# Optimization experiments

Measured on AMD Instinct MI355X. Metric: run time of the kernel, lower is better.

Reference implementation:

```python
import jax, jax.numpy as jnp
import numpy as np

DEG = [1, 72, 201, 816, 1790, 3756, 6923, 12768, 20286, 31710, 51623, 82296, 124280, 177576, 251115, 326064, 395760, 456840, 506179, 516200, 507003, 493746, 489256, 453936, 420025, 411320, 427761, 420700, 420500, 426780, 414284, 407008, 394053, 360910, 322245, 313704, 282902, 270940, 237783, 209000, 193766, 177870, 162110, 144848, 121230, 112700, 93483, 88512, 72275, 80700, 68799, 56784, 42665, 30996, 25630, 12936, 9804, 8584, 5251, 3480, 3111, 2728, 1890, 1472, 1235, 330, 201, 68, 69, 0, 71]
_d = np.array(DEG, dtype=np.float64)
AVG_LOG = float((np.log(np.arange(len(_d)) + 1.0) * _d).sum() / _d.sum())  # avg_deg['log']

N_NODES, N_EDGES, N_GRAPHS = 10000, 100000, 64
TOWERS, F, F_OUT, N_LAYERS = 5, 75, 15, 4


def setup_inputs() -> dict:
    key = jax.random.key(0)
    ks = jax.random.split(key, 32)
    r = lambda i, shape: jax.random.normal(ks[i], shape, jnp.float32) * 0.1
    return {
        "x": jax.random.normal(ks[0], (N_NODES, 14), jnp.float32),
        "edge_index": jax.random.randint(ks[1], (2, N_EDGES), 0, N_NODES, dtype=jnp.int32),
        "edge_attr": jax.random.normal(ks[2], (N_EDGES, 4), jnp.float32),
        "batch": jnp.sort(jax.random.randint(ks[3], (N_NODES,), 0, N_GRAPHS, dtype=jnp.int32)),
        "node_emb_w": r(4, (14, F)), "node_emb_b": r(5, (F,)),
        "edge_emb_w": r(6, (4, 50)), "edge_emb_b": r(7, (50,)),
        "ee_w": r(8, (N_LAYERS, 50, F)), "ee_b": r(9, (N_LAYERS, F)),
        "pre_w": r(10, (N_LAYERS, TOWERS, 3 * F, F)), "pre_b": r(11, (N_LAYERS, TOWERS, F)),
        "post_w": r(12, (N_LAYERS, TOWERS, 13 * F, F_OUT)), "post_b": r(13, (N_LAYERS, TOWERS, F_OUT)),
        "lin_w": r(14, (N_LAYERS, F, F)), "lin_b": r(15, (N_LAYERS, F)),
        "bn_g": jnp.ones((N_LAYERS, F), jnp.float32), "bn_b": jnp.zeros((N_LAYERS, F), jnp.float32),
        "mlp_w1": r(16, (F, 50)), "mlp_b1": r(17, (50,)),
        "mlp_w2": r(18, (50, 25)), "mlp_b2": r(19, (25,)),
        "mlp_w3": r(20, (25, 1)), "mlp_b3": r(21, (1,)),
    }


def _pna_conv(x, src, dst, ea, ee_w, ee_b, pre_w, pre_b, post_w, post_b, lin_w, lin_b):
    # x: [N, F]; ea: [E, edge_dim]; divide_input=False so every tower sees full F.
    N = x.shape[0]
    e = ea @ ee_w + ee_b                                   # edge_encoder  [E, F]
    h = jnp.concatenate([x[dst], x[src], e], axis=-1)       # [x_i, x_j, e] [E, 3F]
    m = jnp.einsum('ef,tfg->etg', h, pre_w) + pre_b         # per-tower pre nn [E, T, F]
    cnt = jax.ops.segment_sum(jnp.ones((m.shape[0],), x.dtype), dst, N)  # in-degree [N]
    cnt1 = jnp.maximum(cnt, 1.0)[:, None, None]
    mean = jax.ops.segment_sum(m, dst, N) / cnt1
    mean_sq = jax.ops.segment_sum(m * m, dst, N) / cnt1
    std = jnp.sqrt(jax.nn.relu(mean_sq - mean * mean) + 1e-5)
    has = (cnt > 0)[:, None, None]
    mn = jnp.where(has, jax.ops.segment_min(m, dst, N), 0.0)
    mx = jnp.where(has, jax.ops.segment_max(m, dst, N), 0.0)
    agg = jnp.concatenate([mean, mn, mx, std], axis=-1)     # [N, T, 4F]
    scl = jnp.log(cnt1 + 1.0) / AVG_LOG                     # amplification scaler
    out = jnp.concatenate([agg, agg * scl, agg / scl], -1)  # identity/amp/atten [N, T, 12F]
    x_rep = jnp.broadcast_to(x[:, None, :], (N, TOWERS, x.shape[1]))
    out = jnp.concatenate([x_rep, out], axis=-1)            # [N, T, 13F]
    out = jnp.einsum('ntf,tfg->ntg', out, post_w) + post_b  # per-tower post nn [N, T, F_out]
    return out.reshape(N, -1) @ lin_w + lin_b               # [N, F]


def _bn(x, g, b):
    mu = x.mean(0)
    var = x.var(0)  # biased, as torch BatchNorm1d uses for normalization
    return (x - mu) * jax.lax.rsqrt(var + 1e-5) * g + b


def reference(x, edge_index, edge_attr, batch, node_emb_w, node_emb_b, edge_emb_w, edge_emb_b,
              ee_w, ee_b, pre_w, pre_b, post_w, post_b, lin_w, lin_b, bn_g, bn_b,
              mlp_w1, mlp_b1, mlp_w2, mlp_b2, mlp_w3, mlp_b3):
    src, dst = edge_index[0], edge_index[1]
    h = x @ node_emb_w + node_emb_b
    ea = edge_attr @ edge_emb_w + edge_emb_b
    for i in range(N_LAYERS):
        h = jax.nn.relu(_bn(_pna_conv(h, src, dst, ea, ee_w[i], ee_b[i], pre_w[i], pre_b[i],
                                      post_w[i], post_b[i], lin_w[i], lin_b[i]), bn_g[i], bn_b[i]))
    per_atom = h
    g = jax.ops.segment_sum(h, batch, N_GRAPHS)             # global_add_pool [G, F]
    g = jax.nn.relu(g @ mlp_w1 + mlp_b1)
    g = jax.nn.relu(g @ mlp_w2 + mlp_b2)
    g = (g @ mlp_w3 + mlp_b3).reshape(-1)                   # num_out==1 -> view(-1)
    return (g, per_atom)
```

## Files before the change

### kernel.cpp

```cpp
#include <hip/hip_runtime.h>
#include <math.h>

#define NN 10000
#define NE 100000
#define NGR 64
#define NT 5
#define FD 75
#define FOUT 15
#define NLAY 4
#define MAXB 1792

typedef __bf16 bf16;
typedef __bf16 bf16x8 __attribute__((ext_vector_type(8)));
typedef float f32x4 __attribute__((ext_vector_type(4)));

__device__ inline unsigned pk2(float a, float b) {
  bf16 x = (bf16)a, y = (bf16)b;
  unsigned short ux, uy;
  __builtin_memcpy(&ux, &x, 2); __builtin_memcpy(&uy, &y, 2);
  return (unsigned)ux | ((unsigned)uy << 16);
}


__global__ __launch_bounds__(256) void k_node_emb(const float* __restrict__ x,
    const float* __restrict__ w, const float* __restrict__ b, bf16* __restrict__ hbf) {
  int idx = blockIdx.x * 256 + threadIdx.x;
  if (idx >= NN * FD) return;
  int n = idx / FD, f = idx - n * FD;
  float acc = b[f];
#pragma unroll
  for (int k = 0; k < 14; ++k) acc += x[n * 14 + k] * w[k * FD + f];
  hbf[n * 80 + f] = (bf16)acc;
}

__global__ __launch_bounds__(256) void k_edge_emb(const float* __restrict__ eattr,
    const float* __restrict__ w, const float* __restrict__ b, bf16* __restrict__ eabf) {
  int idx = blockIdx.x * 256 + threadIdx.x;
  if (idx >= NE * 50) return;
  int e = idx / 50, c = idx - e * 50;
  float acc = b[c];
#pragma unroll
  for (int k = 0; k < 4; ++k) acc += eattr[e * 4 + k] * w[k * 50 + c];
  eabf[e * 56 + c] = (bf16)acc;
}

__global__ __launch_bounds__(256) void k_count(const int* __restrict__ dst, int* __restrict__ deg) {
  int e = blockIdx.x * 256 + threadIdx.x;
  if (e < NE) atomicAdd(&deg[dst[e]], 1);
}

__global__ __launch_bounds__(1024) void k_scan(const int* __restrict__ deg, int* __restrict__ rowptr) {
  __shared__ int buf[1024];
  __shared__ int carry;
  int tid = threadIdx.x;
  if (tid == 0) carry = 0;
  __syncthreads();
  for (int base = 0; base < NN; base += 1024) {
    int i = base + tid;
    int v = (i < NN) ? deg[i] : 0;
    buf[tid] = v;
    __syncthreads();
    for (int off = 1; off < 1024; off <<= 1) {
      int t = (tid >= off) ? buf[tid - off] : 0;
      __syncthreads();
      buf[tid] += t;
      __syncthreads();
    }
    int inc = buf[tid];
    int tot = buf[1023];
    if (i < NN) rowptr[i + 1] = carry + inc;
    __syncthreads();
    if (tid == 0) carry += tot;
    __syncthreads();
  }
  if (tid == 0) rowptr[0] = 0;
}

__global__ __launch_bounds__(256) void k_scl(const int* __restrict__ deg, float* __restrict__ scl,
                                             float* __restrict__ iscl, float inv_avg_log) {
  int n = blockIdx.x * 256 + threadIdx.x;
  if (n >= NN) return;
  float c1 = fmaxf((float)deg[n], 1.f);
  float s = logf(c1 + 1.f) * inv_avg_log;
  scl[n] = s;
  iscl[n] = 1.f / s;
}

__global__ __launch_bounds__(256) void k_scatter(const int* __restrict__ dst, const int* __restrict__ rowptr,
    int* __restrict__ cursor, int* __restrict__ eids) {
  int e = blockIdx.x * 256 + threadIdx.x;
  if (e >= NE) return;
  int d = dst[e];
  int pos = rowptr[d] + atomicAdd(&cursor[d], 1);
  eids[pos] = e;
}

__global__ __launch_bounds__(256) void k_next(const int* __restrict__ rowptr, int* __restrict__ nxt) {
  int n = blockIdx.x * 256 + threadIdx.x;
  if (n >= NN) return;
  int base = rowptr[n];
  int lo = n + 1, hi = min(n + 128, NN);
  while (lo < hi) {
    int mid = (lo + hi + 1) >> 1;
    if (rowptr[mid] - base <= 128) lo = mid; else hi = mid - 1;
  }
  nxt[n] = lo;
}

__global__ __launch_bounds__(1024) void k_walk(const int* __restrict__ nxt,
    int* __restrict__ bstart, int* __restrict__ nblk) {
  __shared__ int lnx[NN];
  int tid = threadIdx.x;
  for (int i = tid; i < NN; i += 1024) lnx[i] = nxt[i];
  __syncthreads();
  if (tid == 0) {
    int b = 0, n = 0;
    while (n < NN && b < MAXB) { bstart[b++] = n; n = lnx[n]; }
    bstart[b] = NN;
    nblk[0] = b;
  }
}


__global__ __launch_bounds__(256) void k_combine(const float* __restrict__ pre_w,
    const float* __restrict__ pre_b, const float* __restrict__ ee_w, const float* __restrict__ ee_b,
    bf16* __restrict__ Wct, float* __restrict__ bc) {
  int idx = blockIdx.x * 256 + threadIdx.x;
  if (idx >= 384 * 256) return;
  int c = idx >> 8, s = idx & 255;
  int t = c / 75, g = c - t * 75;
  int chunk = s >> 6, within = s & 63, sblk = within >> 3, elem = within & 7;
  int lb = sblk ^ (c & 7);
  int k = chunk * 64 + lb * 8 + elem;
  float v = 0.f;
  if (c < 375) {
    if (k < 75)                    v = pre_w[(t * 225 + k) * 75 + g];
    else if (k >= 80 && k < 155)   v = pre_w[(t * 225 + 75 + (k - 80)) * 75 + g];
    else if (k >= 160 && k < 210) {
      int kk = k - 160;
      float a = 0.f;
      for (int f2 = 0; f2 < 75; ++f2) a += ee_w[kk * 75 + f2] * pre_w[(t * 225 + 150 + f2) * 75 + g];
      v = a;
    }
  }
  Wct[c * 256 + s] = (bf16)v;
  if (s == 0) {
    float a = 0.f;
    if (c < 375) {
      a = pre_b[t * 75 + g];
      for (int f2 = 0; f2 < 75; ++f2) a += ee_b[f2] * pre_w[(t * 225 + 150 + f2) * 75 + g];
    }
    bc[c] = a;
  }
}

__global__ __launch_bounds__(256) void k_PL(const float* __restrict__ pw,
    const float* __restrict__ lw, float* __restrict__ PL) {
  int idx = blockIdx.x * 256 + threadIdx.x;
  if (idx >= 5 * 975 * 80) return;
  int t = idx / (975 * 80), rem = idx - t * 975 * 80;
  int row = rem / 80, o = rem - row * 80;
  float v = 0.f;
  if (o < 75) {
#pragma unroll
    for (int j = 0; j < 15; ++j)
      v += pw[((size_t)t * 975 + row) * 15 + j] * lw[(t * 15 + j) * 75 + o];
  }
  PL[idx] = v;
}

__global__ __launch_bounds__(256) void k_combine2b(const float* __restrict__ PL,
    bf16* __restrict__ Wct2) {
  int idx = blockIdx.x * 256 + threadIdx.x;
  if (idx >= 256 * 1664) return;
  int c = idx / 1664, s = idx - c * 1664;
  int chunk = s >> 6, within = s & 63, sblk = within >> 3, elem = within & 7;
  int lb = sblk ^ (c & 7);
  int k = chunk * 64 + lb * 8 + elem;
  int g2 = c / 80, o = c - g2 * 80;
  float val = 0.f;
  if (c < 240 && o < 75) {
    if (k < 75) {
      if (g2 == 0) {
#pragma unroll
        for (int t = 0; t < 5; ++t) val += PL[(t * 975 + k) * 80 + o];
      }
    } else if (k >= 80 && k < 1616) {
      int q = k - 80;
      int si = q / 384, cc = q - si * 384;
      if (cc < 375) {
        int t = cc / 75, g = cc - t * 75;
        int row = 75 + g2 * 300 + si * 75 + g;
        val = PL[((size_t)t * 975 + row) * 80 + o];
      }
    }
  }
  Wct2[(size_t)c * 1664 + s] = (bf16)val;
}

__global__ __launch_bounds__(128) void k_zbias(const float* __restrict__ pb,
    const float* __restrict__ lw, const float* __restrict__ lb, float* __restrict__ zb) {
  int o = blockIdx.x * 128 + threadIdx.x;
  if (o >= 80) return;
  float val = 0.f;
  if (o < 75) {
    val = lb[o];
    for (int t = 0; t < 5; ++t)
      for (int j = 0; j < 15; ++j)
        val += pb[t * 15 + j] * lw[(t * 15 + j) * 75 + o];
  }
  zb[o] = val;
}


#define APTR_(g_, pd_, ps_, pe_) \
  ((g_) < 10 ? (pd_) + (g_) * 8 : (g_) < 20 ? (ps_) + ((g_) - 10) * 8 : \
   (g_) < 27 ? (pe_) + ((g_) - 20) * 8 : zerobuf)

#define LOADA(c_) do { int g_ = (c_) * 8 + slb;                \
    pa0 = *(const uint4*)APTR_(g_, pd0, ps0, pe0);             \
    pa1 = *(const uint4*)APTR_(g_, pd1, ps1, pe1);             \
    pa2 = *(const uint4*)APTR_(g_, pd2, ps2, pe2);             \
    pa3 = *(const uint4*)APTR_(g_, pd3, ps3, pe3); } while (0)

#define LOADB(ntb_, c_) do {                                                      \
    const bf16* wp_ = Wct + (size_t)((ntb_) + sr) * 256 + (c_) * 64 + slb * 8;    \
    pq0 = *(const uint4*)(wp_ + 0 * 8192);                                        \
    pq1 = *(const uint4*)(wp_ + 1 * 8192);                                        \
    pq2 = *(const uint4*)(wp_ + 2 * 8192);                                        \
    pq3 = *(const uint4*)(wp_ + 3 * 8192); } while (0)

#define STORE_AB() do { int swz_ = (slb ^ (sr & 7)) << 4;       \
    *(uint4*)(As + (0 * 32 + sr) * 128 + swz_) = pa0;           \
    *(uint4*)(As + (1 * 32 + sr) * 128 + swz_) = pa1;           \
    *(uint4*)(As + (2 * 32 + sr) * 128 + swz_) = pa2;           \
    *(uint4*)(As + (3 * 32 + sr) * 128 + swz_) = pa3;           \
    *(uint4*)(Bs + (0 * 32 + sr) * 128 + (slb << 4)) = pq0;     \
    *(uint4*)(Bs + (1 * 32 + sr) * 128 + (slb << 4)) = pq1;     \
    *(uint4*)(Bs + (2 * 32 + sr) * 128 + (slb << 4)) = pq2;     \
    *(uint4*)(Bs + (3 * 32 + sr) * 128 + (slb << 4)) = pq3; } while (0)

__global__ __launch_bounds__(256) void k_pre_fused(
    const bf16* __restrict__ hbf, const bf16* __restrict__ eabf,
    const int* __restrict__ eids, const int* __restrict__ srcA, const int* __restrict__ dstA,
    const int* __restrict__ rowptr, const int* __restrict__ bstart, const int* __restrict__ nblk,
    const bf16* __restrict__ Wct, const float* __restrict__ bc,
    const bf16* __restrict__ zerobuf, bf16* __restrict__ aggbf2) {
  __shared__ __align__(16) unsigned char smem[33792];
  unsigned char* As = smem;
  unsigned char* Bs = smem + 16384;
  bf16* m_lds = (bf16*)smem;
  __shared__ const bf16* pDl[128];
  __shared__ const bf16* pSl[128];
  __shared__ const bf16* pEl[128];
  __shared__ int nodeRows[129];
  __shared__ int nq[5];

  const int b = blockIdx.x;
  if (b >= nblk[0]) return;
  const int ntb = blockIdx.y * 128;
  const int tid = threadIdx.x;
  const int n0b = bstart[b], n1b = bstart[b + 1];
  const int rbase = rowptr[n0b];
  const int nrows = rowptr[n1b] - rbase;
  const int nnod = n1b - n0b;

  if (tid == 0) { nq[0] = 0; nq[1] = 0; nq[2] = 0; nq[3] = 0; nq[4] = nnod; }
  if (tid < 128) {
    if (tid < nrows) {
      int e = eids[rbase + tid];
      pDl[tid] = hbf + dstA[e] * 80;
      pSl[tid] = hbf + srcA[e] * 80;
      pEl[tid] = eabf + e * 56;
    } else { pDl[tid] = zerobuf; pSl[tid] = zerobuf; pEl[tid] = zerobuf; }
  }
  if (tid <= nnod) nodeRows[tid] = rowptr[n0b + tid] - rbase;
  __syncthreads();
  if (tid < nnod) {
#pragma unroll
    for (int q = 1; q <= 3; ++q) {
      int target = (nrows * q) >> 2;
      if (nodeRows[tid] < target && nodeRows[tid + 1] >= target) nq[q] = tid + 1;
    }
  }

  const int lane = tid & 63;
  const int wave = tid >> 6;
  const int wr = wave >> 1, wc = wave & 1;
  const int l15 = lane & 15, l4 = lane >> 4;
  const int sr = tid >> 3, slb = tid & 7;

  const bf16 *pd0 = pDl[sr],      *ps0 = pSl[sr],      *pe0 = pEl[sr];
  const bf16 *pd1 = pDl[32 + sr], *ps1 = pSl[32 + sr], *pe1 = pEl[32 + sr];
  const bf16 *pd2 = pDl[64 + sr], *ps2 = pSl[64 + sr], *pe2 = pEl[64 + sr];
  const bf16 *pd3 = pDl[96 + sr], *ps3 = pSl[96 + sr], *pe3 = pEl[96 + sr];

  f32x4 acc[4][4];
  f32x4 zv = {0.f, 0.f, 0.f, 0.f};
#pragma unroll
  for (int i = 0; i < 4; ++i)
#pragma unroll
    for (int j = 0; j < 4; ++j) acc[i][j] = zv;

  uint4 pa0, pa1, pa2, pa3, pq0, pq1, pq2, pq3;
  LOADA(0); LOADB(ntb, 0);

#pragma unroll
  for (int c = 0; c < 4; ++c) {
    STORE_AB();
    __syncthreads();
    if (c < 3) { LOADA(c + 1); LOADB(ntb, c + 1); }
#pragma unroll
    for (int kk = 0; kk < 2; ++kk) {
      int kb = kk * 4 + l4;
      bf16x8 af[4], bfv[4];
#pragma unroll
      for (int i = 0; i < 4; ++i) {
        int row = wr * 64 + i * 16 + l15;
        af[i] = *(const bf16x8*)(As + row * 128 + ((kb ^ (row & 7)) << 4));
      }
#pragma unroll
      for (int j = 0; j < 4; ++j) {
        int col = wc * 64 + j * 16 + l15;
        bfv[j] = *(const bf16x8*)(Bs + col * 128 + ((kb ^ (col & 7)) << 4));
      }
#pragma unroll
      for (int i = 0; i < 4; ++i)
#pragma unroll
        for (int j = 0; j < 4; ++j)
          acc[i][j] = __builtin_amdgcn_mfma_f32_16x16x32_bf16(af[i], bfv[j], acc[i][j], 0, 0, 0);
    }
    __syncthreads();
  }

  float bcv[4];
#pragma unroll
  for (int j = 0; j < 4; ++j) bcv[j] = bc[ntb + wc * 64 + j * 16 + l15];
#pragma unroll
  for (int i = 0; i < 4; ++i) {
    int R = wr * 64 + i * 16 + l4 * 4;
#pragma unroll
    for (int j = 0; j < 4; ++j) {
      int col = wc * 64 + j * 16 + l15;
#pragma unroll
      for (int q = 0; q < 4; ++q)
        m_lds[(R + q) * 132 + col] = (bf16)(acc[i][j][q] + bcv[j]);
    }
  }
  __syncthreads();

  {
    const int cp = tid & 63;
    const int qq = tid >> 6;
    const unsigned char* mb = (const unsigned char*)m_lds;
    for (int i = nq[qq]; i < nq[qq + 1]; ++i) {
      int ra = nodeRows[i], rb2 = nodeRows[i + 1];
      float s0 = 0.f, q0 = 0.f, a0 = INFINITY, b0 = -INFINITY;
      float s1 = 0.f, q1 = 0.f, a1 = INFINITY, b1 = -INFINITY;
      for (int r = ra; r < rb2; ++r) {
        unsigned u = *(const unsigned*)(mb + r * 264 + cp * 4);
        float v0 = __uint_as_float(u << 16);
        float v1 = __uint_as_float(u & 0xffff0000u);
        s0 += v0; q0 += v0 * v0; a0 = fminf(a0, v0); b0 = fmaxf(b0, v0);
        s1 += v1; q1 += v1 * v1; a1 = fminf(a1, v1); b1 = fmaxf(b1, v1);
      }
      int d = rb2 - ra;
      float inv = 1.f / ((d > 0) ? (float)d : 1.f);
      float m0 = s0 * inv, m1 = s1 * inv;
      float sd0 = sqrtf(fmaxf(q0 * inv - m0 * m0, 0.f) + 1e-5f);
      float sd1 = sqrtf(fmaxf(q1 * inv - m1 * m1, 0.f) + 1e-5f);
      if (d == 0) { a0 = 0.f; b0 = 0.f; a1 = 0.f; b1 = 0.f; }
      bf16* ag = aggbf2 + (size_t)(n0b + i) * 1536 + ntb + cp * 2;
      *(unsigned*)(ag)        = pk2(m0, m1);
      *(unsigned*)(ag + 384)  = pk2(a0, a1);
      *(unsigned*)(ag + 768)  = pk2(b0, b1);
      *(unsigned*)(ag + 1152) = pk2(sd0, sd1);
    }
  }
}


#define APG_(g_) ((nA >= NN || (g_) >= 202) ? zerobuf : \
    ((g_) < 10 ? hbf + nA * 80 + (g_) * 8 : aggbf2 + (size_t)nA * 1536 + ((g_) - 10) * 8))

#define LOADP4(c_) do {                                                 \
    int gA_ = (c_) * 16 + slb;                                          \
    pa0 = *(const uint4*)APG_(gA_);                                     \
    pa1 = *(const uint4*)APG_(gA_ + 8);                                 \
    int ko_ = (c_) * 128 + slb * 8;                                     \
    pb0 = *(const uint4*)(pc0 + ko_);                                   \
    pb1 = *(const uint4*)(pc0 + ko_ + 64);                              \
    pb2 = *(const uint4*)(pc1 + ko_);                                   \
    pb3 = *(const uint4*)(pc1 + ko_ + 64);                              \
    pb4 = *(const uint4*)(pc2 + ko_);                                   \
    pb5 = *(const uint4*)(pc2 + ko_ + 64);                              \
    pb6 = *(const uint4*)(pc3 + ko_);                                   \
    pb7 = *(const uint4*)(pc3 + ko_ + 64);                              \
  } while (0)

__global__ __launch_bounds__(256) void k_post4(const bf16* __restrict__ hbf,
    const bf16* __restrict__ aggbf2, const bf16* __restrict__ Wct2,
    const float* __restrict__ zb, const float* __restrict__ scl, const float* __restrict__ iscl,
    const bf16* __restrict__ zerobuf, float* __restrict__ z, float* __restrict__ stat_raw_l) {
  __shared__ __align__(16) unsigned char smem[40960];
  unsigned char* As = smem;
  unsigned char* Bs = smem + 8192;
  float* Ps = (float*)smem;
  __shared__ float sclS[32], isclS[32];
  const int n0 = blockIdx.x * 32;
  const int y  = blockIdx.y;
  const int tid = threadIdx.x;
  const int lane = tid & 63, wave = tid >> 6;
  const int l15 = lane & 15, l4 = lane >> 4;
  const int sr = tid >> 3, slb = tid & 7;
  const int nA = n0 + sr;

  const bf16 *pc0, *pc1, *pc2, *pc3;
  {
    int c0 = sr, c1 = sr + 32, c2 = sr + 64, c3 = sr + 96;
    int l0 = (c0 / 40) * 80 + y * 40 + (c0 % 40);
    int l1 = (c1 / 40) * 80 + y * 40 + (c1 % 40);
    int l2 = (c2 / 40) * 80 + y * 40 + (c2 % 40);
    int l3 = (c3 < 120) ? ((c3 / 40) * 80 + y * 40 + (c3 % 40)) : 0;
    pc0 = Wct2 + (size_t)l0 * 1664;
    pc1 = Wct2 + (size_t)l1 * 1664;
    pc2 = Wct2 + (size_t)l2 * 1664;
    pc3 = Wct2 + (size_t)l3 * 1664;
  }
  if (tid < 32) {
    int n = n0 + tid;
    sclS[tid] = (n < NN) ? scl[n] : 0.f;
    isclS[tid] = (n < NN) ? iscl[n] : 0.f;
  }

  f32x4 acc[2][2];
  f32x4 zvv = {0.f, 0.f, 0.f, 0.f};
#pragma unroll
  for (int i = 0; i < 2; ++i)
#pragma unroll
    for (int j = 0; j < 2; ++j) acc[i][j] = zvv;

  uint4 pa0, pa1, pb0, pb1, pb2, pb3, pb4, pb5, pb6, pb7;
  LOADP4(0);
  for (int c = 0; c < 13; ++c) {
    {
      int s1_ = (slb ^ (sr & 7)) << 4;
      *(uint4*)(As + sr * 256 + s1_) = pa0;
      *(uint4*)(As + sr * 256 + s1_ + 128) = pa1;
      *(uint4*)(Bs + (sr)      * 256 + (slb << 4)) = pb0;
      *(uint4*)(Bs + (sr)      * 256 + (slb << 4) + 128) = pb1;
      *(uint4*)(Bs + (sr + 32) * 256 + (slb << 4)) = pb2;
      *(uint4*)(Bs + (sr + 32) * 256 + (slb << 4) + 128) = pb3;
      *(uint4*)(Bs + (sr + 64) * 256 + (slb << 4)) = pb4;
      *(uint4*)(Bs + (sr + 64) * 256 + (slb << 4) + 128) = pb5;
      *(uint4*)(Bs + (sr + 96) * 256 + (slb << 4)) = pb6;
      *(uint4*)(Bs + (sr + 96) * 256 + (slb << 4) + 128) = pb7;
    }
    __syncthreads();
    if (c < 12) LOADP4(c + 1);
#pragma unroll
    for (int kk = 0; kk < 4; ++kk) {
      int kb = kk * 4 + l4;
      bf16x8 af[2], bv[2];
#pragma unroll
      for (int i = 0; i < 2; ++i) {
        int row = i * 16 + l15;
        af[i] = *(const bf16x8*)(As + row * 256 + (((kb & 8) | ((kb & 7) ^ (row & 7))) << 4));
      }
#pragma unroll
      for (int j = 0; j < 2; ++j) {
        int cidx = wave * 32 + j * 16 + l15;
        bv[j] = *(const bf16x8*)(Bs + cidx * 256 + (((kb & 8) | ((kb & 7) ^ (cidx & 7))) << 4));
      }
#pragma unroll
      for (int i = 0; i < 2; ++i)
#pragma unroll
        for (int j = 0; j < 2; ++j)
          acc[i][j] = __builtin_amdgcn_mfma_f32_16x16x32_bf16(af[i], bv[j], acc[i][j], 0, 0, 0);
    }
    __syncthreads();
  }

#pragma unroll
  for (int i = 0; i < 2; ++i) {
#pragma unroll
    for (int j = 0; j < 2; ++j) {
      int cidx = wave * 32 + j * 16 + l15;
#pragma unroll
      for (int q = 0; q < 4; ++q)
        Ps[(i * 16 + l4 * 4 + q) * 132 + cidx] = acc[i][j][q];
    }
  }
  __syncthreads();

  float v0_, v1_, v2_, v3_, v4_;
  int r0_, r1_, r2_, r3_, r4_, f0_, f1_, f2_, f3_, f4_;
#define EPI(t_, vv_, rr_, ff_) do {                                           \
    int idx_ = tid + (t_) * 256;                                              \
    rr_ = idx_ / 40; ff_ = idx_ - rr_ * 40;                                   \
    int n_ = n0 + rr_, zc_ = y * 40 + ff_;                                    \
    float v_ = 0.f;                                                           \
    if (n_ < NN && zc_ < 75) {                                                \
      v_ = Ps[rr_ * 132 + ff_] + sclS[rr_] * Ps[rr_ * 132 + 40 + ff_]         \
         + isclS[rr_] * Ps[rr_ * 132 + 80 + ff_] + zb[zc_];                   \
      z[n_ * 75 + zc_] = v_;                                                  \
    }                                                                         \
    vv_ = v_;                                                                 \
  } while (0)
  EPI(0, v0_, r0_, f0_); EPI(1, v1_, r1_, f1_); EPI(2, v2_, r2_, f2_);
  EPI(3, v3_, r3_, f3_); EPI(4, v4_, r4_, f4_);
#undef EPI
  __syncthreads();
  Ps[r0_ * 132 + f0_] = v0_;
  Ps[r1_ * 132 + f1_] = v1_;
  Ps[r2_ * 132 + f2_] = v2_;
  Ps[r3_ * 132 + f3_] = v3_;
  Ps[r4_ * 132 + f4_] = v4_;
  __syncthreads();
  if (tid < 40) {
    int zc = y * 40 + tid;
    if (zc < 75) {
      float s = 0.f, s2 = 0.f;
#pragma unroll
      for (int r = 0; r < 32; ++r) {
        float v = Ps[r * 132 + tid];
        s += v; s2 += v * v;
      }
      atomicAdd(&stat_raw_l[zc], s);
      atomicAdd(&stat_raw_l[75 + zc], s2);
    }
  }
}

__global__ __launch_bounds__(256) void k_bnapply(const float* __restrict__ z,
    const float* __restrict__ stat_raw, const float* __restrict__ g, const float* __restrict__ b,
    float* __restrict__ outF, bf16* __restrict__ hbf) {
  int idx = blockIdx.x * 256 + threadIdx.x;
  if (idx >= NN * FD) return;
  int n = idx / FD, f = idx - n * FD;
  float mu = stat_raw[f] * (1.f / NN);
  float var = stat_raw[75 + f] * (1.f / NN) - mu * mu;
  var = fmaxf(var, 0.f);
  float rs = 1.f / sqrtf(var + 1e-5f);
  float v = (z[idx] - mu) * rs * g[f] + b[f];
  v = fmaxf(v, 0.f);
  if (outF) outF[idx] = v;
  hbf[n * 80 + f] = (bf16)v;
}

__global__ __launch_bounds__(256) void k_pool(const float* __restrict__ h, const int* __restrict__ batch,
                                              float* __restrict__ gpool) {
  int idx = blockIdx.x * 256 + threadIdx.x;
  if (idx >= NN * FD) return;
  int n = idx / FD, f = idx - n * FD;
  atomicAdd(&gpool[batch[n] * FD + f], h[idx]);
}

__global__ __launch_bounds__(256) void k_mlp(const float* __restrict__ gpool,
    const float* __restrict__ w1, const float* __restrict__ b1,
    const float* __restrict__ w2, const float* __restrict__ b2,
    const float* __restrict__ w3, const float* __restrict__ b3,
    float* __restrict__ out) {
  __shared__ float G[NGR * FD];
  __shared__ float G1[NGR * 50];
  __shared__ float G2[NGR * 25];
  int tid = threadIdx.x;
  for (int i = tid; i < NGR * FD; i += 256) G[i] = gpool[i];
  __syncthreads();
  for (int i = tid; i < NGR * 50; i += 256) {
    int r = i / 50, c = i - r * 50;
    float a = b1[c];
    for (int k = 0; k < FD; ++k) a += G[r * FD + k] * w1[k * 50 + c];
    G1[i] = fmaxf(a, 0.f);
  }
  __syncthreads();
  for (int i = tid; i < NGR * 25; i += 256) {
    int r = i / 25, c = i - r * 25;
    float a = b2[c];
    for (int k = 0; k < 50; ++k) a += G1[r * 50 + k] * w2[k * 25 + c];
    G2[i] = fmaxf(a, 0.f);
  }
  __syncthreads();
  if (tid < NGR) {
    float a = b3[0];
    for (int k = 0; k < 25; ++k) a += G2[tid * 25 + k] * w3[k];
    out[tid] = a;
  }
}


extern "C" void kernel_launch(void* const* d_in, const int* in_sizes, int n_in,
                              void* d_out, int out_size, void* d_ws, size_t ws_size,
                              hipStream_t stream) {
  (void)in_sizes; (void)n_in; (void)out_size; (void)ws_size;
  const float* x      = (const float*)d_in[0];
  const int*   eidx   = (const int*)  d_in[1];
  const float* eattr  = (const float*)d_in[2];
  const int*   batch  = (const int*)  d_in[3];
  const float* nw     = (const float*)d_in[4];
  const float* nb     = (const float*)d_in[5];
  const float* ew     = (const float*)d_in[6];
  const float* ebias  = (const float*)d_in[7];
  const float* ee_w   = (const float*)d_in[8];
  const float* ee_b   = (const float*)d_in[9];
  const float* pre_w  = (const float*)d_in[10];
  const float* pre_b  = (const float*)d_in[11];
  const float* post_w = (const float*)d_in[12];
  const float* post_b = (const float*)d_in[13];
  const float* lin_w  = (const float*)d_in[14];
  const float* lin_b  = (const float*)d_in[15];
  const float* bn_g   = (const float*)d_in[16];
  const float* bn_b   = (const float*)d_in[17];
  const float* w1 = (const float*)d_in[18];
  const float* b1 = (const float*)d_in[19];
  const float* w2 = (const float*)d_in[20];
  const float* b2 = (const float*)d_in[21];
  const float* w3 = (const float*)d_in[22];
  const float* b3 = (const float*)d_in[23];

  const int* srcA = eidx;
  const int* dstA = eidx + NE;

  char* base = (char*)d_ws;
  size_t off = 0;
  auto alloc = [&](size_t bytes) -> char* {
    char* p = base + off;
    off = (off + bytes + 255) & ~(size_t)255;
    return p;
  };
  bf16*  hbf    = (bf16*) alloc((size_t)NN * 80 * 2);
  bf16*  eabf   = (bf16*) alloc((size_t)NE * 56 * 2);
  bf16*  aggbf2 = (bf16*) alloc((size_t)NN * 1536 * 2);
  float* z      = (float*)alloc((size_t)NN * FD * 4);
  bf16*  WctA   = (bf16*) alloc((size_t)NLAY * 384 * 256 * 2);
  float* bcA    = (float*)alloc((size_t)NLAY * 384 * 4);
  bf16*  Wct2A  = (bf16*) alloc((size_t)NLAY * 256 * 1664 * 2);
  float* zbA    = (float*)alloc((size_t)NLAY * 80 * 4);
  float* PL     = (float*)alloc((size_t)5 * 975 * 80 * 4);
  float* scl    = (float*)alloc(NN * 4);
  float* iscl   = (float*)alloc(NN * 4);
  int*   deg    = (int*)alloc(NN * 4);
  int*   rowptr = (int*)alloc((NN + 1) * 4);
  int*   cursor = (int*)alloc(NN * 4);
  int*   eids   = (int*)alloc(NE * 4);
  int*   nxt    = (int*)alloc(NN * 4);
  int*   bstart = (int*)alloc((MAXB + 1) * 4);
  int*   nblk   = (int*)alloc(16);
  float* stat_all = (float*)alloc((size_t)NLAY * 160 * 4);
  float* gpool  = (float*)alloc(NGR * FD * 4);
  bf16*  zerobuf = (bf16*)alloc(256);

  static const int DEG_TAB[71] = {1, 72, 201, 816, 1790, 3756, 6923, 12768, 20286, 31710,
    51623, 82296, 124280, 177576, 251115, 326064, 395760, 456840, 506179, 516200, 507003,
    493746, 489256, 453936, 420025, 411320, 427761, 420700, 420500, 426780, 414284, 407008,
    394053, 360910, 322245, 313704, 282902, 270940, 237783, 209000, 193766, 177870, 162110,
    144848, 121230, 112700, 93483, 88512, 72275, 80700, 68799, 56784, 42665, 30996, 25630,
    12936, 9804, 8584, 5251, 3480, 3111, 2728, 1890, 1472, 1235, 330, 201, 68, 69, 0, 71};
  double num = 0.0, den = 0.0;
  for (int i = 0; i < 71; ++i) { num += log((double)i + 1.0) * DEG_TAB[i]; den += DEG_TAB[i]; }
  float inv_avg_log = (float)(den / num);

  hipMemsetAsync(deg, 0, NN * 4, stream);
  hipMemsetAsync(cursor, 0, NN * 4, stream);
  hipMemsetAsync(gpool, 0, NGR * FD * 4, stream);
  hipMemsetAsync(stat_all, 0, (size_t)NLAY * 160 * 4, stream);
  hipMemsetAsync(zerobuf, 0, 256, stream);

  k_node_emb<<<(NN * FD + 255) / 256, 256, 0, stream>>>(x, nw, nb, hbf);
  k_edge_emb<<<(NE * 50 + 255) / 256, 256, 0, stream>>>(eattr, ew, ebias, eabf);
  k_count<<<(NE + 255) / 256, 256, 0, stream>>>(dstA, deg);
  k_scan<<<1, 1024, 0, stream>>>(deg, rowptr);
  k_scl<<<(NN + 255) / 256, 256, 0, stream>>>(deg, scl, iscl, inv_avg_log);
  k_scatter<<<(NE + 255) / 256, 256, 0, stream>>>(dstA, rowptr, cursor, eids);
  k_next<<<(NN + 255) / 256, 256, 0, stream>>>(rowptr, nxt);
  k_walk<<<1, 1024, 0, stream>>>(nxt, bstart, nblk);

  for (int l = 0; l < NLAY; ++l) {
    k_combine<<<384, 256, 0, stream>>>(
        pre_w + (size_t)l * NT * 225 * FD, pre_b + (size_t)l * NT * FD,
        ee_w + (size_t)l * 50 * FD, ee_b + (size_t)l * FD,
        WctA + (size_t)l * 384 * 256, bcA + (size_t)l * 384);
    k_PL<<<(5 * 975 * 80 + 255) / 256, 256, 0, stream>>>(
        post_w + (size_t)l * NT * 975 * FOUT, lin_w + (size_t)l * FD * FD, PL);
    k_combine2b<<<(256 * 1664 + 255) / 256, 256, 0, stream>>>(PL, Wct2A + (size_t)l * 256 * 1664);
    k_zbias<<<1, 128, 0, stream>>>(post_b + (size_t)l * NT * FOUT,
        lin_w + (size_t)l * FD * FD, lin_b + (size_t)l * FD, zbA + (size_t)l * 80);
  }

  float* outp = (float*)d_out;
  for (int l = 0; l < NLAY; ++l) {
    dim3 gpref(MAXB, 3);
    k_pre_fused<<<gpref, 256, 0, stream>>>(hbf, eabf, eids, srcA, dstA, rowptr, bstart, nblk,
        WctA + (size_t)l * 384 * 256, bcA + (size_t)l * 384, zerobuf, aggbf2);
    dim3 gpost((NN + 31) / 32, 2);
    k_post4<<<gpost, 256, 0, stream>>>(hbf, aggbf2, Wct2A + (size_t)l * 256 * 1664,
        zbA + (size_t)l * 80, scl, iscl, zerobuf, z, stat_all + (size_t)l * 160);
    float* wdst = (l == NLAY - 1) ? (outp + NGR) : nullptr;
    k_bnapply<<<(NN * FD + 255) / 256, 256, 0, stream>>>(z, stat_all + (size_t)l * 160,
        bn_g + (size_t)l * FD, bn_b + (size_t)l * FD, wdst, hbf);
  }

  k_pool<<<(NN * FD + 255) / 256, 256, 0, stream>>>(outp + NGR, batch, gpool);
  k_mlp<<<1, 256, 0, stream>>>(gpool, w1, b1, w2, b2, w3, b3, outp);
}
```

Baseline: 604.1 us.

## Drop LDS staging in pre-aggregation GEMM and load MFMA fragments from global

```diff
diff --git a/kernel.cpp b/kernel.cpp
--- a/kernel.cpp
+++ b/kernel.cpp
@@ -154,6 +154,26 @@
   }
 }
 
+__global__ __launch_bounds__(256) void k_combined(const float* __restrict__ pre_w,
+    const float* __restrict__ ee_w, bf16* __restrict__ Wctd) {
+  int idx = blockIdx.x * 256 + threadIdx.x;
+  if (idx >= 384 * 256) return;
+  int c = idx >> 8, k = idx & 255;
+  int t = c / 75, g = c - t * 75;
+  float v = 0.f;
+  if (c < 375) {
+    if (k < 75)                    v = pre_w[(t * 225 + k) * 75 + g];
+    else if (k >= 80 && k < 155)   v = pre_w[(t * 225 + 75 + (k - 80)) * 75 + g];
+    else if (k >= 160 && k < 210) {
+      int kk = k - 160;
+      float a = 0.f;
+      for (int f2 = 0; f2 < 75; ++f2) a += ee_w[kk * 75 + f2] * pre_w[(t * 225 + 150 + f2) * 75 + g];
+      v = a;
+    }
+  }
+  Wctd[c * 256 + k] = (bf16)v;
+}
+
 __global__ __launch_bounds__(256) void k_PL(const float* __restrict__ pw,
     const float* __restrict__ lw, float* __restrict__ PL) {
   int idx = blockIdx.x * 256 + threadIdx.x;
@@ -217,39 +237,13 @@
   ((g_) < 10 ? (pd_) + (g_) * 8 : (g_) < 20 ? (ps_) + ((g_) - 10) * 8 : \
    (g_) < 27 ? (pe_) + ((g_) - 20) * 8 : zerobuf)
 
-#define LOADA(c_) do { int g_ = (c_) * 8 + slb;                \
-    pa0 = *(const uint4*)APTR_(g_, pd0, ps0, pe0);             \
-    pa1 = *(const uint4*)APTR_(g_, pd1, ps1, pe1);             \
-    pa2 = *(const uint4*)APTR_(g_, pd2, ps2, pe2);             \
-    pa3 = *(const uint4*)APTR_(g_, pd3, ps3, pe3); } while (0)
-
-#define LOADB(ntb_, c_) do {                                                      \
-    const bf16* wp_ = Wct + (size_t)((ntb_) + sr) * 256 + (c_) * 64 + slb * 8;    \
-    pq0 = *(const uint4*)(wp_ + 0 * 8192);                                        \
-    pq1 = *(const uint4*)(wp_ + 1 * 8192);                                        \
-    pq2 = *(const uint4*)(wp_ + 2 * 8192);                                        \
-    pq3 = *(const uint4*)(wp_ + 3 * 8192); } while (0)
-
-#define STORE_AB() do { int swz_ = (slb ^ (sr & 7)) << 4;       \
-    *(uint4*)(As + (0 * 32 + sr) * 128 + swz_) = pa0;           \
-    *(uint4*)(As + (1 * 32 + sr) * 128 + swz_) = pa1;           \
-    *(uint4*)(As + (2 * 32 + sr) * 128 + swz_) = pa2;           \
-    *(uint4*)(As + (3 * 32 + sr) * 128 + swz_) = pa3;           \
-    *(uint4*)(Bs + (0 * 32 + sr) * 128 + (slb << 4)) = pq0;     \
-    *(uint4*)(Bs + (1 * 32 + sr) * 128 + (slb << 4)) = pq1;     \
-    *(uint4*)(Bs + (2 * 32 + sr) * 128 + (slb << 4)) = pq2;     \
-    *(uint4*)(Bs + (3 * 32 + sr) * 128 + (slb << 4)) = pq3; } while (0)
-
 __global__ __launch_bounds__(256) void k_pre_fused(
     const bf16* __restrict__ hbf, const bf16* __restrict__ eabf,
     const int* __restrict__ eids, const int* __restrict__ srcA, const int* __restrict__ dstA,
     const int* __restrict__ rowptr, const int* __restrict__ bstart, const int* __restrict__ nblk,
-    const bf16* __restrict__ Wct, const float* __restrict__ bc,
+    const bf16* __restrict__ Wctd, const float* __restrict__ bc,
     const bf16* __restrict__ zerobuf, bf16* __restrict__ aggbf2) {
-  __shared__ __align__(16) unsigned char smem[33792];
-  unsigned char* As = smem;
-  unsigned char* Bs = smem + 16384;
-  bf16* m_lds = (bf16*)smem;
+  __shared__ bf16 m_lds[128 * 132];
   __shared__ const bf16* pDl[128];
   __shared__ const bf16* pSl[128];
   __shared__ const bf16* pEl[128];
@@ -285,66 +279,68 @@
   }
 
   const int lane = tid & 63;
-  const int wave = tid >> 6;
-  const int wr = wave >> 1, wc = wave & 1;
+  const int w = tid >> 6;
   const int l15 = lane & 15, l4 = lane >> 4;
-  const int sr = tid >> 3, slb = tid & 7;
-
-  const bf16 *pd0 = pDl[sr],      *ps0 = pSl[sr],      *pe0 = pEl[sr];
-  const bf16 *pd1 = pDl[32 + sr], *ps1 = pSl[32 + sr], *pe1 = pEl[32 + sr];
-  const bf16 *pd2 = pDl[64 + sr], *ps2 = pSl[64 + sr], *pe2 = pEl[64 + sr];
-  const bf16 *pd3 = pDl[96 + sr], *ps3 = pSl[96 + sr], *pe3 = pEl[96 + sr];
-
-  f32x4 acc[4][4];
+
+  const bf16 *pd0 = pDl[w * 32 + l15],      *ps0 = pSl[w * 32 + l15],      *pe0 = pEl[w * 32 + l15];
+  const bf16 *pd1 = pDl[w * 32 + 16 + l15], *ps1 = pSl[w * 32 + 16 + l15], *pe1 = pEl[w * 32 + 16 + l15];
+
+  float bcv[8];
+#pragma unroll
+  for (int j = 0; j < 8; ++j) bcv[j] = bc[ntb + j * 16 + l15];
+
+  f32x4 acc[2][8];
   f32x4 zv = {0.f, 0.f, 0.f, 0.f};
 #pragma unroll
-  for (int i = 0; i < 4; ++i)
-#pragma unroll
-    for (int j = 0; j < 4; ++j) acc[i][j] = zv;
-
-  uint4 pa0, pa1, pa2, pa3, pq0, pq1, pq2, pq3;
-  LOADA(0); LOADB(ntb, 0);
-
-#pragma unroll
+  for (int i = 0; i < 2; ++i)
+#pragma unroll
+    for (int j = 0; j < 8; ++j) acc[i][j] = zv;
+
+  const bf16* wbase = Wctd + (size_t)(ntb + l15) * 256;
+
   for (int c = 0; c < 4; ++c) {
-    STORE_AB();
-    __syncthreads();
-    if (c < 3) { LOADA(c + 1); LOADB(ntb, c + 1); }
 #pragma unroll
     for (int kk = 0; kk < 2; ++kk) {
-      int kb = kk * 4 + l4;
-      bf16x8 af[4], bfv[4];
-#pragma unroll
-      for (int i = 0; i < 4; ++i) {
-        int row = wr * 64 + i * 16 + l15;
-        af[i] = *(const bf16x8*)(As + row * 128 + ((kb ^ (row & 7)) << 4));
+      int g = c * 8 + kk * 4 + l4;
+      bf16x8 a0 = *(const bf16x8*)APTR_(g, pd0, ps0, pe0);
+      bf16x8 a1 = *(const bf16x8*)APTR_(g, pd1, ps1, pe1);
+      int ko = c * 64 + (kk * 4 + l4) * 8;
+      bf16x8 bv0 = *(const bf16x8*)(wbase + 0 * 4096 + ko);
+      bf16x8 bv1 = *(const bf16x8*)(wbase + 1 * 4096 + ko);
+      bf16x8 bv2 = *(const bf16x8*)(wbase + 2 * 4096 + ko);
+      bf16x8 bv3 = *(const bf16x8*)(wbase + 3 * 4096 + ko);
+      bf16x8 bv4 = *(const bf16x8*)(wbase + 4 * 4096 + ko);
+      bf16x8 bv5 = *(const bf16x8*)(wbase + 5 * 4096 + ko);
+      bf16x8 bv6 = *(const bf16x8*)(wbase + 6 * 4096 + ko);
+      bf16x8 bv7 = *(const bf16x8*)(wbase + 7 * 4096 + ko);
+      acc[0][0] = __builtin_amdgcn_mfma_f32_16x16x32_bf16(a0, bv0, acc[0][0], 0, 0, 0);
+      acc[1][0] = __builtin_amdgcn_mfma_f32_16x16x32_bf16(a1, bv0, acc[1][0], 0, 0, 0);
+      acc[0][1] = __builtin_amdgcn_mfma_f32_16x16x32_bf16(a0, bv1, acc[0][1], 0, 0, 0);
+      acc[1][1] = __builtin_amdgcn_mfma_f32_16x16x32_bf16(a1, bv1, acc[1][1], 0, 0, 0);
+      acc[0][2] = __builtin_amdgcn_mfma_f32_16x16x32_bf16(a0, bv2, acc[0][2], 0, 0, 0);
+      acc[1][2] = __builtin_amdgcn_mfma_f32_16x16x32_bf16(a1, bv2, acc[1][2], 0, 0, 0);
+      acc[0][3] = __builtin_amdgcn_mfma_f32_16x16x32_bf16(a0, bv3, acc[0][3], 0, 0, 0);
+      acc[1][3] = __builtin_amdgcn_mfma_f32_16x16x32_bf16(a1, bv3, acc[1][3], 0, 0, 0);
+      acc[0][4] = __builtin_amdgcn_mfma_f32_16x16x32_bf16(a0, bv4, acc[0][4], 0, 0, 0);
+      acc[1][4] = __builtin_amdgcn_mfma_f32_16x16x32_bf16(a1, bv4, acc[1][4], 0, 0, 0);
+      acc[0][5] = __builtin_amdgcn_mfma_f32_16x16x32_bf16(a0, bv5, acc[0][5], 0, 0, 0);
+      acc[1][5] = __builtin_amdgcn_mfma_f32_16x16x32_bf16(a1, bv5, acc[1][5], 0, 0, 0);
+      acc[0][6] = __builtin_amdgcn_mfma_f32_16x16x32_bf16(a0, bv6, acc[0][6], 0, 0, 0);
+      acc[1][6] = __builtin_amdgcn_mfma_f32_16x16x32_bf16(a1, bv6, acc[1][6], 0, 0, 0);
+      acc[0][7] = __builtin_amdgcn_mfma_f32_16x16x32_bf16(a0, bv7, acc[0][7], 0, 0, 0);
+      acc[1][7] = __builtin_amdgcn_mfma_f32_16x16x32_bf16(a1, bv7, acc[1][7], 0, 0, 0);
+    }
+  }
+
+#pragma unroll
+  for (int i = 0; i < 2; ++i) {
+#pragma unroll
+    for (int j = 0; j < 8; ++j) {
+#pragma unroll
+      for (int q = 0; q < 4; ++q) {
+        int R = w * 32 + i * 16 + l4 * 4 + q;
+        m_lds[R * 132 + j * 16 + l15] = (bf16)(acc[i][j][q] + bcv[j]);
       }
-#pragma unroll
-      for (int j = 0; j < 4; ++j) {
-        int col = wc * 64 + j * 16 + l15;
-        bfv[j] = *(const bf16x8*)(Bs + col * 128 + ((kb ^ (col & 7)) << 4));
-      }
-#pragma unroll
-      for (int i = 0; i < 4; ++i)
-#pragma unroll
-        for (int j = 0; j < 4; ++j)
-          acc[i][j] = __builtin_amdgcn_mfma_f32_16x16x32_bf16(af[i], bfv[j], acc[i][j], 0, 0, 0);
-    }
-    __syncthreads();
-  }
-
-  float bcv[4];
-#pragma unroll
-  for (int j = 0; j < 4; ++j) bcv[j] = bc[ntb + wc * 64 + j * 16 + l15];
-#pragma unroll
-  for (int i = 0; i < 4; ++i) {
-    int R = wr * 64 + i * 16 + l4 * 4;
-#pragma unroll
-    for (int j = 0; j < 4; ++j) {
-      int col = wc * 64 + j * 16 + l15;
-#pragma unroll
-      for (int q = 0; q < 4; ++q)
-        m_lds[(R + q) * 132 + col] = (bf16)(acc[i][j][q] + bcv[j]);
     }
   }
   __syncthreads();
@@ -632,7 +628,7 @@
   bf16*  eabf   = (bf16*) alloc((size_t)NE * 56 * 2);
   bf16*  aggbf2 = (bf16*) alloc((size_t)NN * 1536 * 2);
   float* z      = (float*)alloc((size_t)NN * FD * 4);
-  bf16*  WctA   = (bf16*) alloc((size_t)NLAY * 384 * 256 * 2);
+  bf16*  WctdA  = (bf16*) alloc((size_t)NLAY * 384 * 256 * 2);
   float* bcA    = (float*)alloc((size_t)NLAY * 384 * 4);
   bf16*  Wct2A  = (bf16*) alloc((size_t)NLAY * 256 * 1664 * 2);
   float* zbA    = (float*)alloc((size_t)NLAY * 80 * 4);
@@ -649,6 +645,7 @@
   float* stat_all = (float*)alloc((size_t)NLAY * 160 * 4);
   float* gpool  = (float*)alloc(NGR * FD * 4);
   bf16*  zerobuf = (bf16*)alloc(256);
+  bf16*  WctScratch = (bf16*)alloc((size_t)384 * 256 * 2);
 
   static const int DEG_TAB[71] = {1, 72, 201, 816, 1790, 3756, 6923, 12768, 20286, 31710,
     51623, 82296, 124280, 177576, 251115, 326064, 395760, 456840, 506179, 516200, 507003,
@@ -679,7 +676,10 @@
     k_combine<<<384, 256, 0, stream>>>(
         pre_w + (size_t)l * NT * 225 * FD, pre_b + (size_t)l * NT * FD,
         ee_w + (size_t)l * 50 * FD, ee_b + (size_t)l * FD,
-        WctA + (size_t)l * 384 * 256, bcA + (size_t)l * 384);
+        WctScratch, bcA + (size_t)l * 384);
+    k_combined<<<384, 256, 0, stream>>>(
+        pre_w + (size_t)l * NT * 225 * FD, ee_w + (size_t)l * 50 * FD,
+        WctdA + (size_t)l * 384 * 256);
     k_PL<<<(5 * 975 * 80 + 255) / 256, 256, 0, stream>>>(
         post_w + (size_t)l * NT * 975 * FOUT, lin_w + (size_t)l * FD * FD, PL);
     k_combine2b<<<(256 * 1664 + 255) / 256, 256, 0, stream>>>(PL, Wct2A + (size_t)l * 256 * 1664);
@@ -691,7 +691,7 @@
   for (int l = 0; l < NLAY; ++l) {
     dim3 gpref(MAXB, 3);
     k_pre_fused<<<gpref, 256, 0, stream>>>(hbf, eabf, eids, srcA, dstA, rowptr, bstart, nblk,
-        WctA + (size_t)l * 384 * 256, bcA + (size_t)l * 384, zerobuf, aggbf2);
+        WctdA + (size_t)l * 384 * 256, bcA + (size_t)l * 384, zerobuf, aggbf2);
     dim3 gpost((NN + 31) / 32, 2);
     k_post4<<<gpost, 256, 0, stream>>>(hbf, aggbf2, Wct2A + (size_t)l * 256 * 1664,
         zbA + (size_t)l * 80, scl, iscl, zerobuf, z, stat_all + (size_t)l * 160);
```

Result: slower. 838.2 us (+38.8%).
